# Kernel optimization log

Measured on AMD Instinct MI355X. Metric: run time of the kernel, lower is better.

## Reference

```python
import jax, jax.numpy as jnp
import numpy as np

N, E = 50000, 800000
IN_FEATS, HIDDEN, HEADS, NUM_CLASSES, EDGE_FEAT = 64, 64, 4, 4, 2
D_HEAD = HIDDEN // HEADS


def _lin(key, fan_in, fan_out):
    k1, k2 = jax.random.split(key)
    s = 1.0 / np.sqrt(fan_in)
    W = jax.random.uniform(k1, (fan_in, fan_out), jnp.float32, -s, s)
    b = jax.random.uniform(k2, (fan_out,), jnp.float32, -s, s)
    return W, b


def setup_inputs() -> dict:
    key = jax.random.key(0)
    ks = jax.random.split(key, 10)
    x = jax.random.normal(ks[0], (N, IN_FEATS), jnp.float32)
    edge_index = jax.random.randint(ks[1], (2, E), 0, N, jnp.int32)
    edge_attr = jax.random.normal(ks[2], (E, EDGE_FEAT), jnp.float32)
    Wn, bn = _lin(ks[3], IN_FEATS, HIDDEN)
    We, be = _lin(ks[4], EDGE_FEAT, HIDDEN)
    Wq, bq = _lin(ks[5], HIDDEN, HIDDEN)
    Wk, bk = _lin(ks[6], HIDDEN, HIDDEN)
    Wv, bv = _lin(ks[7], HIDDEN, HIDDEN)
    Ws, bs = _lin(ks[8], HIDDEN, HIDDEN)   # lin_skip (root weight)
    Wf, bf = _lin(ks[9], HIDDEN, NUM_CLASSES)
    return {"x": x, "edge_index": edge_index, "edge_attr": edge_attr,
            "Wn": Wn, "bn": bn, "We": We, "be": be,
            "Wq": Wq, "bq": bq, "Wk": Wk, "bk": bk, "Wv": Wv, "bv": bv,
            "Ws": Ws, "bs": bs, "Wf": Wf, "bf": bf}


def _segment_softmax(logits, seg, num_segments):
    # logits: [E, H], seg: [E] destination node ids
    m = jax.ops.segment_max(logits, seg, num_segments=num_segments)  # [N, H]
    m = jnp.where(jnp.isfinite(m), m, 0.0)
    e = jnp.exp(logits - m[seg])
    s = jax.ops.segment_sum(e, seg, num_segments=num_segments)
    return e / (s[seg] + 1e-16)


def reference(x, edge_index, edge_attr, Wn, bn, We, be, Wq, bq, Wk, bk, Wv, bv, Ws, bs, Wf, bf):
    src, dst = edge_index[0], edge_index[1]
    h = x @ Wn + bn                                   # [N, HIDDEN]
    ea = (edge_attr @ We + be).reshape(E, HEADS, D_HEAD)
    q = (h @ Wq + bq).reshape(N, HEADS, D_HEAD)
    k = (h @ Wk + bk).reshape(N, HEADS, D_HEAD)
    v = (h @ Wv + bv).reshape(N, HEADS, D_HEAD)
    # per-edge attention logits (PyG flow source_to_target: query at dst, key at src)
    logits = jnp.einsum('ehd,ehd->eh', q[dst], k[src]) / np.sqrt(D_HEAD)
    alpha = _segment_softmax(logits, dst, N)          # [E, H]
    # edge_attr added to values (lin_edge is None since edge_dim not set)
    msg = (v[src] + ea) * alpha[:, :, None]           # [E, H, D]
    out = jax.ops.segment_sum(msg, dst, num_segments=N).reshape(N, HIDDEN)
    out = out + h @ Ws + bs                           # root/skip connection
    # dropout is identity in eval mode
    edge_out = out[src] + out[dst]                    # [E, HIDDEN]
    return edge_out @ Wf + bf                         # [E, NUM_CLASSES]
```

## Files before the change

kernel.cpp:

```cpp
#include <hip/hip_runtime.h>
#include <hip/hip_bf16.h>
#include <hip/hip_fp16.h>

#define N_NODES 50000
#define N_EDGES 800000
#define NB_T64 ((N_NODES + 63) / 64)
#define WT_BLOCKS 16
#define CAP 64

#define BIN_SHIFT 8
#define NBINS ((N_NODES + 255) / 256)
#define CAP_BIN 5120
#define EPB 2048
#define NB_BIN ((N_EDGES + EPB - 1) / EPB)

typedef unsigned short u16;
typedef unsigned int   u32;
typedef __attribute__((ext_vector_type(8))) short short8;
typedef __attribute__((ext_vector_type(4))) float f32x4;

__device__ __forceinline__ float bf2f(u16 u) {
    union { u32 i; float f; } z; z.i = ((u32)u) << 16; return z.f;
}
__device__ __forceinline__ u16 f2bf(float f) {
    union { float f; u32 i; } z; z.f = f;
    u32 x = z.i;
    u32 r = (x + 0x7fffu + ((x >> 16) & 1u)) >> 16;
    return (u16)r;
}
__device__ __forceinline__ float ldf(const void* p, size_t i, bool isbf) {
    return isbf ? bf2f(((const u16*)p)[i]) : ((const float*)p)[i];
}
__device__ __forceinline__ u16 ldbf(const void* p, size_t i, bool isbf) {
    return isbf ? ((const u16*)p)[i] : f2bf(((const float*)p)[i]);
}

#define WSB_COUNT 772

__global__ __launch_bounds__(256) void k_init(
    const void* __restrict__ Wn, const void* __restrict__ bn,
    const void* __restrict__ Wq, const void* __restrict__ bq,
    const void* __restrict__ Wk, const void* __restrict__ bk,
    const void* __restrict__ Wv, const void* __restrict__ bv,
    const void* __restrict__ Ws, const void* __restrict__ bs,
    const void* __restrict__ We, const void* __restrict__ be,
    const void* __restrict__ Wf, const void* __restrict__ bfv,
    const int* __restrict__ ei, const void* __restrict__ ea,
    u16* __restrict__ wsT, float* __restrict__ wsB,
    uint2* __restrict__ bins, u32* __restrict__ gcur,
    const int isbf)
{
    const int t = threadIdx.x, bid = blockIdx.x;
    if (bid >= WT_BLOCKS) {
        __shared__ u32 h[NBINS];
        __shared__ u32 off[NBINS];
        const int blk = bid - WT_BLOCKS;
        const int e0 = blk * EPB + t * 8;
        const bool vec = (e0 + 8 <= N_EDGES);
        int dv[8];
        if (vec) {
            const int4 a = *(const int4*)(ei + N_EDGES + e0);
            const int4 b = *(const int4*)(ei + N_EDGES + e0 + 4);
            dv[0] = a.x; dv[1] = a.y; dv[2] = a.z; dv[3] = a.w;
            dv[4] = b.x; dv[5] = b.y; dv[6] = b.z; dv[7] = b.w;
        } else {
            #pragma unroll
            for (int j = 0; j < 8; ++j)
                dv[j] = (e0 + j < N_EDGES) ? ei[N_EDGES + e0 + j] : -1;
        }
        if (t < NBINS) { h[t] = 0; off[t] = 0; }
        __syncthreads();
        #pragma unroll
        for (int j = 0; j < 8; ++j)
            if (dv[j] >= 0) atomicAdd(&h[dv[j] >> BIN_SHIFT], 1u);
        __syncthreads();
        if (t < NBINS && h[t] != 0) h[t] = atomicAdd(&gcur[t], h[t]);
        __syncthreads();
        int sv[8];
        if (vec) {
            const int4 a = *(const int4*)(ei + e0);
            const int4 b = *(const int4*)(ei + e0 + 4);
            sv[0] = a.x; sv[1] = a.y; sv[2] = a.z; sv[3] = a.w;
            sv[4] = b.x; sv[5] = b.y; sv[6] = b.z; sv[7] = b.w;
        } else {
            #pragma unroll
            for (int j = 0; j < 8; ++j)
                sv[j] = (e0 + j < N_EDGES) ? ei[e0 + j] : 0;
        }
        #pragma unroll
        for (int j = 0; j < 8; ++j) {
            if (dv[j] < 0) continue;
            const int e = e0 + j;
            float ea0, ea1;
            if (isbf) {
                const u32 w2 = ((const u32*)ea)[e];
                ea0 = bf2f((u16)(w2 & 0xffffu));
                ea1 = bf2f((u16)(w2 >> 16));
            } else {
                const float2 f2 = ((const float2*)ea)[e];
                ea0 = f2.x; ea1 = f2.y;
            }
            const __half2 hh = __floats2half2_rn(ea0, ea1);
            const int b = dv[j] >> BIN_SHIFT;
            const u32 rank = atomicAdd(&off[b], 1u);
            const u32 slot = h[b] + rank;
            if (slot < CAP_BIN) {
                uint2 r;
                r.x = (u32)sv[j] | ((u32)dv[j] << 16);
                r.y = *(const u32*)&hh;
                bins[(size_t)b * CAP_BIN + slot] = r;
            }
        }
        return;
    }

    const int i = bid * 256 + t;
    {
        const int kk = i >> 6, n = i & 63;
        const int o = n * 64 + kk;
        wsT[0 * 4096 + o] = ldbf(Wn, i, isbf);
        wsT[1 * 4096 + o] = ldbf(Wq, i, isbf);
        wsT[2 * 4096 + o] = ldbf(Wk, i, isbf);
        wsT[3 * 4096 + o] = ldbf(Wv, i, isbf);
        wsT[4 * 4096 + o] = ldbf(Ws, i, isbf);
    }
    if (bid == 0) {
        if (t < 64) {
            wsB[t]       = ldf(bn, t, isbf);
            wsB[64 + t]  = ldf(bq, t, isbf);
            wsB[128 + t] = ldf(bk, t, isbf);
            wsB[192 + t] = ldf(bv, t, isbf);
            wsB[256 + t] = ldf(bs, t, isbf);
            wsB[320 + t] = ldf(We, t, isbf);
            wsB[384 + t] = ldf(We, 64 + t, isbf);
            wsB[448 + t] = ldf(be, t, isbf);
        }
        wsB[512 + t] = ldf(Wf, t, isbf);
        if (t < 4) wsB[768 + t] = ldf(bfv, t, isbf);
    }
}

__global__ __launch_bounds__(512, 4) void k_bn(
    const void* __restrict__ x,
    const u16* __restrict__ wsT, const float* __restrict__ wsB,
    const uint2* __restrict__ bins, const u32* __restrict__ gcur,
    int* __restrict__ deg, uint2* __restrict__ rec,
    u16* __restrict__ qbf, u16* __restrict__ kbf, u16* __restrict__ vbf,
    u16* __restrict__ obf, const int isbf)
{
    __shared__ u16 xs[2 * 32 * 72];
    const int t = threadIdx.x, bid = blockIdx.x;

    if (bid < NBINS) {
        __shared__ u32 cnt[1 << BIN_SHIFT];
        const int lo = bid << BIN_SHIFT;
        const int rsz = (N_NODES - lo < (1 << BIN_SHIFT)) ? (N_NODES - lo)
                                                          : (1 << BIN_SHIFT);
        for (int i = t; i < (1 << BIN_SHIFT); i += 512) cnt[i] = 0;
        __syncthreads();
        int n = (int)gcur[bid];
        if (n > CAP_BIN) n = CAP_BIN;
        const uint2* bp = bins + (size_t)bid * CAP_BIN;
        for (int i = t; i < n; i += 512) {
            const uint2 r = bp[i];
            const u32 d = r.x >> 16;
            const u32 rank = atomicAdd(&cnt[d - (u32)lo], 1u) & (u32)(CAP - 1);
            uint2 o;
            o.x = r.x & 0xffffu;
            o.y = r.y;
            rec[((size_t)d << 6) + rank] = o;
        }
        __syncthreads();
        for (int i = t; i < rsz; i += 512) deg[lo + i] = (int)cnt[i];
        return;
    }

    const int tt = t & 255, half = t >> 8;
    const int w = tt >> 6, lane = tt & 63;
    const int l15 = lane & 15, quad = lane >> 4;
    const int base = (bid - NBINS) * 64 + half * 32;
    u16* xh = xs + half * (32 * 72);

    {
        const int m = tt >> 3, kc = tt & 7;
        const int node = base + m;
        short8 vd = {0, 0, 0, 0, 0, 0, 0, 0};
        if (node < N_NODES) {
            if (isbf) {
                vd = *(const short8*)((const u16*)x + (size_t)node * 64 + kc * 8);
            } else {
                const float4 f0 = *(const float4*)((const float*)x + (size_t)node * 64 + kc * 8);
                const float4 f1 = *(const float4*)((const float*)x + (size_t)node * 64 + kc * 8 + 4);
                vd[0] = f2bf(f0.x); vd[1] = f2bf(f0.y);
                vd[2] = f2bf(f0.z); vd[3] = f2bf(f0.w);
                vd[4] = f2bf(f1.x); vd[5] = f2bf(f1.y);
                vd[6] = f2bf(f1.z); vd[7] = f2bf(f1.w);
            }
        }
        *(short8*)(xh + m * 72 + kc * 8) = vd;
    }
    short8 b1[2][4];
    if (w < 2) {
        #pragma unroll
        for (int ks = 0; ks < 2; ++ks)
            #pragma unroll
            for (int nt = 0; nt < 4; ++nt)
                b1[ks][nt] = *(const short8*)(wsT + (nt * 16 + l15) * 64 + ks * 32 + quad * 8);
    }
    __syncthreads();

    if (w < 2) {
        f32x4 acc1[4];
        #pragma unroll
        for (int nt = 0; nt < 4; ++nt) acc1[nt] = (f32x4){0.f, 0.f, 0.f, 0.f};
        #pragma unroll
        for (int ks = 0; ks < 2; ++ks) {
            const short8 a = *(const short8*)(xh + (w * 16 + l15) * 72 + ks * 32 + quad * 8);
            #pragma unroll
            for (int nt = 0; nt < 4; ++nt)
                acc1[nt] = __builtin_amdgcn_mfma_f32_16x16x32_bf16(a, b1[ks][nt], acc1[nt], 0, 0, 0);
        }
        #pragma unroll
        for (int nt = 0; nt < 4; ++nt)
            #pragma unroll
            for (int r = 0; r < 4; ++r) {
                const int m = w * 16 + quad * 4 + r;
                const int col = nt * 16 + l15;
                xh[m * 72 + col] = f2bf(acc1[nt][r] + wsB[col]);
            }
    }
    short8 b2[2][4];
    {
        const u16* wt = wsT + (w + 1) * 4096;
        #pragma unroll
        for (int ks = 0; ks < 2; ++ks)
            #pragma unroll
            for (int nt = 0; nt < 4; ++nt)
                b2[ks][nt] = *(const short8*)(wt + (nt * 16 + l15) * 64 + ks * 32 + quad * 8);
    }
    __syncthreads();

    {
        f32x4 acc2[2][4];
        #pragma unroll
        for (int mt = 0; mt < 2; ++mt)
            #pragma unroll
            for (int nt = 0; nt < 4; ++nt) acc2[mt][nt] = (f32x4){0.f, 0.f, 0.f, 0.f};
        #pragma unroll
        for (int ks = 0; ks < 2; ++ks) {
            short8 a[2];
            #pragma unroll
            for (int mt = 0; mt < 2; ++mt)
                a[mt] = *(const short8*)(xh + (mt * 16 + l15) * 72 + ks * 32 + quad * 8);
            #pragma unroll
            for (int nt = 0; nt < 4; ++nt)
                #pragma unroll
                for (int mt = 0; mt < 2; ++mt)
                    acc2[mt][nt] = __builtin_amdgcn_mfma_f32_16x16x32_bf16(a[mt], b2[ks][nt], acc2[mt][nt], 0, 0, 0);
        }
        const float* bias = wsB + 64 + w * 64;
        u16* outp = (w == 0) ? qbf : (w == 1) ? kbf : (w == 2) ? vbf : obf;
        #pragma unroll
        for (int mt = 0; mt < 2; ++mt)
            #pragma unroll
            for (int nt = 0; nt < 4; ++nt)
                #pragma unroll
                for (int r = 0; r < 4; ++r) {
                    const int node = base + mt * 16 + quad * 4 + r;
                    if (node >= N_NODES) continue;
                    const int col = nt * 16 + l15;
                    outp[(size_t)node * 64 + col] = f2bf(acc2[mt][nt][r] + bias[col]);
                }
    }
}

__global__ __launch_bounds__(256) void k_agg(
    const int* __restrict__ deg,
    const uint2* __restrict__ rec,
    const u16* __restrict__ qbf, const u16* __restrict__ kbf,
    const u16* __restrict__ vbf, const u16* __restrict__ obf,
    const float* __restrict__ wsB,
    float4* __restrict__ y)
{
    const int wid = (blockIdx.x * 256 + threadIdx.x) >> 6;
    const int lane = threadIdx.x & 63;
    if (wid >= N_NODES) return;
    const int d = wid;
    const int lg = lane & 15;
    const int g  = lane >> 4;

    const ushort4 q4u = *(const ushort4*)(qbf + (size_t)d * 64 + lg * 4);
    const float q0 = bf2f(q4u.x), q1 = bf2f(q4u.y);
    const float q2 = bf2f(q4u.z), q3 = bf2f(q4u.w);

    const int beg = d << 6;
    int dg = deg[d];
    dg = (dg > CAP) ? CAP : dg;

    float den = 0.f, sa0 = 0.f, sa1 = 0.f;
    float av0 = 0.f, av1 = 0.f, av2 = 0.f, av3 = 0.f;

    if (dg > 0) {
        const u16* kp = kbf + lg * 4;
        const u16* vp = vbf + lg * 4;
        uint2 rn = rec[beg + g];
        for (int j = 0; j < dg; j += 4) {
            const uint2 r = rn;
            const int nb = (j + 4 < dg) ? (beg + j + 4) : (beg + j);
            rn = rec[nb + g];
            const bool valid = (j + g) < dg;
            const u32 rx = valid ? r.x : 0u;
            const u32 ry = valid ? r.y : 0u;
            const size_t off = (size_t)rx * 64;
            const ushort4 k4 = *(const ushort4*)(kp + off);
            const ushort4 v4 = *(const ushort4*)(vp + off);
            float prod = q0 * bf2f(k4.x) + q1 * bf2f(k4.y)
                       + q2 * bf2f(k4.z) + q3 * bf2f(k4.w);
            prod += __shfl_xor(prod, 1, 64);
            prod += __shfl_xor(prod, 2, 64);
            float ex = __expf(prod * 0.25f);
            ex = valid ? ex : 0.f;
            const float2 eaf = __half22float2(*(const __half2*)&ry);
            den += ex;
            sa0 += ex * eaf.x;
            sa1 += ex * eaf.y;
            av0 += ex * bf2f(v4.x);
            av1 += ex * bf2f(v4.y);
            av2 += ex * bf2f(v4.z);
            av3 += ex * bf2f(v4.w);
        }
    }
    #pragma unroll
    for (int o = 16; o < 64; o <<= 1) {
        den += __shfl_xor(den, o, 64);
        sa0 += __shfl_xor(sa0, o, 64);
        sa1 += __shfl_xor(sa1, o, 64);
        av0 += __shfl_xor(av0, o, 64);
        av1 += __shfl_xor(av1, o, 64);
        av2 += __shfl_xor(av2, o, 64);
        av3 += __shfl_xor(av3, o, 64);
    }

    const float4 we04 = *(const float4*)(wsB + 320 + lg * 4);
    const float4 we14 = *(const float4*)(wsB + 384 + lg * 4);
    const float4 bef4 = *(const float4*)(wsB + 448 + lg * 4);
    const ushort4 o4 = *(const ushort4*)(obf + (size_t)d * 64 + lg * 4);
    const float rden = 1.0f / (den + 1e-16f);
    const float res0 = bf2f(o4.x) + (av0 + we04.x * sa0 + we14.x * sa1 + bef4.x * den) * rden;
    const float res1 = bf2f(o4.y) + (av1 + we04.y * sa0 + we14.y * sa1 + bef4.y * den) * rden;
    const float res2 = bf2f(o4.z) + (av2 + we04.z * sa0 + we14.z * sa1 + bef4.z * den) * rden;
    const float res3 = bf2f(o4.w) + (av3 + we04.w * sa0 + we14.w * sa1 + bef4.w * den) * rden;

    const float4 wf0 = *(const float4*)(wsB + 512 + (lg * 4 + 0) * 4);
    const float4 wf1 = *(const float4*)(wsB + 512 + (lg * 4 + 1) * 4);
    const float4 wf2 = *(const float4*)(wsB + 512 + (lg * 4 + 2) * 4);
    const float4 wf3 = *(const float4*)(wsB + 512 + (lg * 4 + 3) * 4);
    float y0 = res0 * wf0.x + res1 * wf1.x + res2 * wf2.x + res3 * wf3.x;
    float y1 = res0 * wf0.y + res1 * wf1.y + res2 * wf2.y + res3 * wf3.y;
    float y2 = res0 * wf0.z + res1 * wf1.z + res2 * wf2.z + res3 * wf3.z;
    float y3 = res0 * wf0.w + res1 * wf1.w + res2 * wf2.w + res3 * wf3.w;
    #pragma unroll
    for (int o = 1; o < 16; o <<= 1) {
        y0 += __shfl_xor(y0, o, 64);
        y1 += __shfl_xor(y1, o, 64);
        y2 += __shfl_xor(y2, o, 64);
        y3 += __shfl_xor(y3, o, 64);
    }
    if (lane == 0) {
        float4 yv;
        yv.x = y0 + 0.5f * wsB[768];
        yv.y = y1 + 0.5f * wsB[769];
        yv.z = y2 + 0.5f * wsB[770];
        yv.w = y3 + 0.5f * wsB[771];
        y[d] = yv;
    }
}

__global__ __launch_bounds__(256) void k_edgeout(
    const int* __restrict__ ei,
    const float4* __restrict__ y,
    void* __restrict__ out, const int isbf)
{
    const int idx = blockIdx.x * 256 + threadIdx.x;
    const int e0 = idx * 2;
    if (e0 >= N_EDGES) return;
    const int2 ss = *(const int2*)(ei + e0);
    const int2 dd = *(const int2*)(ei + N_EDGES + e0);
    const float4 ya = y[ss.x], yb = y[dd.x];
    const float4 yc = y[ss.y], yd = y[dd.y];
    const float a0 = ya.x + yb.x, a1 = ya.y + yb.y;
    const float a2 = ya.z + yb.z, a3 = ya.w + yb.w;
    const float c0 = yc.x + yd.x, c1 = yc.y + yd.y;
    const float c2 = yc.z + yd.z, c3 = yc.w + yd.w;
    if (isbf) {
        uint4 r;
        r.x = (u32)f2bf(a0) | ((u32)f2bf(a1) << 16);
        r.y = (u32)f2bf(a2) | ((u32)f2bf(a3) << 16);
        r.z = (u32)f2bf(c0) | ((u32)f2bf(c1) << 16);
        r.w = (u32)f2bf(c2) | ((u32)f2bf(c3) << 16);
        *(uint4*)((u16*)out + (size_t)e0 * 4) = r;
    } else {
        float4 r0; r0.x = a0; r0.y = a1; r0.z = a2; r0.w = a3;
        float4 r1; r1.x = c0; r1.y = c1; r1.z = c2; r1.w = c3;
        *(float4*)((float*)out + (size_t)e0 * 4) = r0;
        *(float4*)((float*)out + (size_t)e0 * 4 + 4) = r1;
    }
}

extern "C" void kernel_launch(void* const* d_in, const int* in_sizes, int n_in,
                              void* d_out, int out_size, void* d_ws, size_t ws_size,
                              hipStream_t stream)
{
    (void)n_in; (void)out_size; (void)ws_size;
    const void* x   = d_in[0];
    const int*  ei  = (const int*)d_in[1];
    const void* ea  = d_in[2];
    const void* Wn  = d_in[3];  const void* bn  = d_in[4];
    const void* We  = d_in[5];  const void* be  = d_in[6];
    const void* Wq  = d_in[7];  const void* bq  = d_in[8];
    const void* Wk  = d_in[9];  const void* bk  = d_in[10];
    const void* Wv  = d_in[11]; const void* bv  = d_in[12];
    const void* Ws_ = d_in[13]; const void* bs  = d_in[14];
    const void* Wf  = d_in[15]; const void* bfv = d_in[16];

    const int isbf = (in_sizes[0] == N_NODES * 64 * 2) ? 1 : 0;

    char*   wsp   = (char*)d_ws;
    uint2*  rec   = (uint2*)wsp;
    float4* y     = (float4*)(rec + (size_t)N_NODES * CAP);
    u16*    qbf   = (u16*)(y + N_NODES);
    u16*    kbf   = qbf + (size_t)N_NODES * 64;
    u16*    vbf   = kbf + (size_t)N_NODES * 64;
    u16*    obf   = vbf + (size_t)N_NODES * 64;
    u16*    wsT   = obf + (size_t)N_NODES * 64;
    float*  wsB   = (float*)(wsT + 5 * 4096);
    int*    deg   = (int*)(wsB + WSB_COUNT);
    uint2*  bins  = (uint2*)(deg + N_NODES);
    u32*    gcur  = (u32*)(bins + (size_t)NBINS * CAP_BIN);

    hipMemsetAsync(gcur, 0, NBINS * sizeof(u32), stream);
    k_init<<<WT_BLOCKS + NB_BIN, 256, 0, stream>>>(
        Wn, bn, Wq, bq, Wk, bk, Wv, bv, Ws_, bs, We, be, Wf, bfv, ei, ea,
        wsT, wsB, bins, gcur, isbf);
    k_bn<<<NBINS + NB_T64, 512, 0, stream>>>(x, wsT, wsB, bins, gcur,
                                             deg, rec, qbf, kbf, vbf, obf, isbf);
    k_agg<<<(N_NODES * 64 + 255) / 256, 256, 0, stream>>>(deg, rec, qbf, kbf,
                                                          vbf, obf, wsB, y);
    k_edgeout<<<(N_EDGES / 2 + 255) / 256, 256, 0, stream>>>(ei, y, d_out, isbf);
}
```

Before: 201.9 us.

## Interleave K and V rows and batch edge gathers in aggregation

K and V projections are now stored interleaved per node, four K values followed by four V values per lane slot, so each lane fetches both with one 16-byte load instead of two 8-byte loads. The aggregation loop now handles 16 edges per iteration. It issues four record loads and four KV gathers up front to expose more memory-level parallelism, and the skip-connection load is hoisted to the start. The cost is scattered 2-byte writes in the projection kernel and more registers per thread, and the record reads past the node's degree rely on the 64-slot capacity.

```diff
diff --git a/kernel.cpp b/kernel.cpp
--- a/kernel.cpp
+++ b/kernel.cpp
@@ -17,6 +17,7 @@
 typedef unsigned short u16;
 typedef unsigned int   u32;
 typedef __attribute__((ext_vector_type(8))) short short8;
+typedef __attribute__((ext_vector_type(8))) unsigned short ushort8;
 typedef __attribute__((ext_vector_type(4))) float f32x4;
 
 __device__ __forceinline__ float bf2f(u16 u) {
@@ -145,7 +146,7 @@
     const u16* __restrict__ wsT, const float* __restrict__ wsB,
     const uint2* __restrict__ bins, const u32* __restrict__ gcur,
     int* __restrict__ deg, uint2* __restrict__ rec,
-    u16* __restrict__ qbf, u16* __restrict__ kbf, u16* __restrict__ vbf,
+    u16* __restrict__ qbf, u16* __restrict__ kvbf,
     u16* __restrict__ obf, const int isbf)
 {
     __shared__ u16 xs[2 * 32 * 72];
@@ -259,7 +260,6 @@
                     acc2[mt][nt] = __builtin_amdgcn_mfma_f32_16x16x32_bf16(a[mt], b2[ks][nt], acc2[mt][nt], 0, 0, 0);
         }
         const float* bias = wsB + 64 + w * 64;
-        u16* outp = (w == 0) ? qbf : (w == 1) ? kbf : (w == 2) ? vbf : obf;
         #pragma unroll
         for (int mt = 0; mt < 2; ++mt)
             #pragma unroll
@@ -269,7 +269,15 @@
                     const int node = base + mt * 16 + quad * 4 + r;
                     if (node >= N_NODES) continue;
                     const int col = nt * 16 + l15;
-                    outp[(size_t)node * 64 + col] = f2bf(acc2[mt][nt][r] + bias[col]);
+                    const u16 val = f2bf(acc2[mt][nt][r] + bias[col]);
+                    if (w == 1) {
+                        kvbf[(size_t)node * 128 + ((col >> 2) << 3) + (col & 3)] = val;
+                    } else if (w == 2) {
+                        kvbf[(size_t)node * 128 + ((col >> 2) << 3) + 4 + (col & 3)] = val;
+                    } else {
+                        u16* outp = (w == 0) ? qbf : obf;
+                        outp[(size_t)node * 64 + col] = val;
+                    }
                 }
     }
 }
@@ -277,8 +285,8 @@
 __global__ __launch_bounds__(256) void k_agg(
     const int* __restrict__ deg,
     const uint2* __restrict__ rec,
-    const u16* __restrict__ qbf, const u16* __restrict__ kbf,
-    const u16* __restrict__ vbf, const u16* __restrict__ obf,
+    const u16* __restrict__ qbf, const u16* __restrict__ kvbf,
+    const u16* __restrict__ obf,
     const float* __restrict__ wsB,
     float4* __restrict__ y)
 {
@@ -290,6 +298,7 @@
     const int g  = lane >> 4;
 
     const ushort4 q4u = *(const ushort4*)(qbf + (size_t)d * 64 + lg * 4);
+    const ushort4 o4  = *(const ushort4*)(obf + (size_t)d * 64 + lg * 4);
     const float q0 = bf2f(q4u.x), q1 = bf2f(q4u.y);
     const float q2 = bf2f(q4u.z), q3 = bf2f(q4u.w);
 
@@ -300,34 +309,37 @@
     float den = 0.f, sa0 = 0.f, sa1 = 0.f;
     float av0 = 0.f, av1 = 0.f, av2 = 0.f, av3 = 0.f;
 
-    if (dg > 0) {
-        const u16* kp = kbf + lg * 4;
-        const u16* vp = vbf + lg * 4;
-        uint2 rn = rec[beg + g];
-        for (int j = 0; j < dg; j += 4) {
-            const uint2 r = rn;
-            const int nb = (j + 4 < dg) ? (beg + j + 4) : (beg + j);
-            rn = rec[nb + g];
-            const bool valid = (j + g) < dg;
-            const u32 rx = valid ? r.x : 0u;
-            const u32 ry = valid ? r.y : 0u;
-            const size_t off = (size_t)rx * 64;
-            const ushort4 k4 = *(const ushort4*)(kp + off);
-            const ushort4 v4 = *(const ushort4*)(vp + off);
-            float prod = q0 * bf2f(k4.x) + q1 * bf2f(k4.y)
-                       + q2 * bf2f(k4.z) + q3 * bf2f(k4.w);
+    const u16* kvp = kvbf + lg * 8;
+    for (int j = 0; j < dg; j += 16) {
+        uint2 rr[4];
+        #pragma unroll
+        for (int qq = 0; qq < 4; ++qq)
+            rr[qq] = rec[beg + j + 4 * qq + g];
+        ushort8 kv[4];
+        #pragma unroll
+        for (int qq = 0; qq < 4; ++qq) {
+            const bool valid = (j + 4 * qq + g) < dg;
+            const u32 rx = valid ? rr[qq].x : 0u;
+            kv[qq] = *(const ushort8*)(kvp + (size_t)rx * 128);
+        }
+        #pragma unroll
+        for (int qq = 0; qq < 4; ++qq) {
+            const bool valid = (j + 4 * qq + g) < dg;
+            float prod = q0 * bf2f(kv[qq][0]) + q1 * bf2f(kv[qq][1])
+                       + q2 * bf2f(kv[qq][2]) + q3 * bf2f(kv[qq][3]);
             prod += __shfl_xor(prod, 1, 64);
             prod += __shfl_xor(prod, 2, 64);
             float ex = __expf(prod * 0.25f);
             ex = valid ? ex : 0.f;
+            const u32 ry = valid ? rr[qq].y : 0u;
             const float2 eaf = __half22float2(*(const __half2*)&ry);
             den += ex;
             sa0 += ex * eaf.x;
             sa1 += ex * eaf.y;
-            av0 += ex * bf2f(v4.x);
-            av1 += ex * bf2f(v4.y);
-            av2 += ex * bf2f(v4.z);
-            av3 += ex * bf2f(v4.w);
+            av0 += ex * bf2f(kv[qq][4]);
+            av1 += ex * bf2f(kv[qq][5]);
+            av2 += ex * bf2f(kv[qq][6]);
+            av3 += ex * bf2f(kv[qq][7]);
         }
     }
     #pragma unroll
@@ -344,7 +356,6 @@
     const float4 we04 = *(const float4*)(wsB + 320 + lg * 4);
     const float4 we14 = *(const float4*)(wsB + 384 + lg * 4);
     const float4 bef4 = *(const float4*)(wsB + 448 + lg * 4);
-    const ushort4 o4 = *(const ushort4*)(obf + (size_t)d * 64 + lg * 4);
     const float rden = 1.0f / (den + 1e-16f);
     const float res0 = bf2f(o4.x) + (av0 + we04.x * sa0 + we14.x * sa1 + bef4.x * den) * rden;
     const float res1 = bf2f(o4.y) + (av1 + we04.y * sa0 + we14.y * sa1 + bef4.y * den) * rden;
@@ -429,9 +440,8 @@
     uint2*  rec   = (uint2*)wsp;
     float4* y     = (float4*)(rec + (size_t)N_NODES * CAP);
     u16*    qbf   = (u16*)(y + N_NODES);
-    u16*    kbf   = qbf + (size_t)N_NODES * 64;
-    u16*    vbf   = kbf + (size_t)N_NODES * 64;
-    u16*    obf   = vbf + (size_t)N_NODES * 64;
+    u16*    kvbf  = qbf + (size_t)N_NODES * 64;
+    u16*    obf   = kvbf + (size_t)N_NODES * 128;
     u16*    wsT   = obf + (size_t)N_NODES * 64;
     float*  wsB   = (float*)(wsT + 5 * 4096);
     int*    deg   = (int*)(wsB + WSB_COUNT);
@@ -443,8 +453,8 @@
         Wn, bn, Wq, bq, Wk, bk, Wv, bv, Ws_, bs, We, be, Wf, bfv, ei, ea,
         wsT, wsB, bins, gcur, isbf);
     k_bn<<<NBINS + NB_T64, 512, 0, stream>>>(x, wsT, wsB, bins, gcur,
-                                             deg, rec, qbf, kbf, vbf, obf, isbf);
-    k_agg<<<(N_NODES * 64 + 255) / 256, 256, 0, stream>>>(deg, rec, qbf, kbf,
-                                                          vbf, obf, wsB, y);
+                                             deg, rec, qbf, kvbf, obf, isbf);
+    k_agg<<<(N_NODES * 64 + 255) / 256, 256, 0, stream>>>(deg, rec, qbf, kvbf,
+                                                          obf, wsB, y);
     k_edgeout<<<(N_EDGES / 2 + 255) / 256, 256, 0, stream>>>(ei, y, d_out, isbf);
 }
```

After: 197.8 us. 1.02x faster.
